# Optimization experiments

Measured on AMD Instinct MI355X. Metric: run time of the kernel, lower is better.

Reference implementation:

```python
import jax, jax.numpy as jnp
import numpy as np

E = 512      # embed_size
H = 8        # num_heads
L = 4        # num_layers
SF = 4       # sparsity_factor
F_IN = 128   # input feature dim (nn.Linear(128, embed_size))
N_CLS = 10


def setup_inputs() -> dict:
    key = jax.random.key(0)
    ks = jax.random.split(key, 14)
    B, S = 8, 1024
    s = 0.02
    inp = {
        "x": jax.random.normal(ks[0], (B, S, F_IN), jnp.float32),
        "emb_w": jax.random.normal(ks[1], (F_IN, E), jnp.float32) * s,
        "emb_b": jnp.zeros((E,), jnp.float32),
        "Wq": jax.random.normal(ks[2], (L, E, E), jnp.float32) * s,
        "Wk": jax.random.normal(ks[3], (L, E, E), jnp.float32) * s,
        "Wv": jax.random.normal(ks[4], (L, E, E), jnp.float32) * s,
        "Wo": jax.random.normal(ks[5], (L, E, E), jnp.float32) * s,
        "bq": jnp.zeros((L, E), jnp.float32),
        "bk": jnp.zeros((L, E), jnp.float32),
        "bv": jnp.zeros((L, E), jnp.float32),
        "bo": jnp.zeros((L, E), jnp.float32),
        "fc_w": jax.random.normal(ks[6], (E, N_CLS), jnp.float32) * s,
        "fc_b": jnp.zeros((N_CLS,), jnp.float32),
    }
    return inp


def _sparse_attn(h, wq, wk, wv, wo, bq, bk, bv, bo):
    # One SparseAttention layer: per-query top-k sparsified multi-head attention.
    B, S, _ = h.shape
    d = E // H
    k = max(1, S // SF)  # keep top S/sparsity_factor keys per query
    scale = 1.0 / np.sqrt(d)

    def heads(t):  # [B,S,E] -> [B,H,S,d]
        return t.reshape(B, S, H, d).transpose(0, 2, 1, 3)

    q = heads(h @ wq + bq)
    kk = heads(h @ wk + bk)
    v = heads(h @ wv + bv)

    scores = jnp.einsum('bhqd,bhkd->bhqk', q, kk) * scale  # [B,H,S,S]
    thresh = jax.lax.top_k(scores, k)[0][..., -1:]          # k-th largest per query
    scores = jnp.where(scores >= thresh, scores, jnp.float32(-1e9))
    p = jax.nn.softmax(scores, axis=-1)
    o = jnp.einsum('bhqk,bhkd->bhqd', p, v)                 # [B,H,S,d]
    o = o.transpose(0, 2, 1, 3).reshape(B, S, E)
    return o @ wo + bo


def reference(x, emb_w, emb_b, Wq, Wk, Wv, Wo, bq, bk, bv, bo, fc_w, fc_b):
    h = x @ emb_w + emb_b  # [B,S,E]
    for l in range(L):
        h = _sparse_attn(h, Wq[l], Wk[l], Wv[l], Wo[l], bq[l], bk[l], bv[l], bo[l])
    return h.mean(axis=1) @ fc_w + fc_b  # [B,10]
```

## Files before the change

### kernel.cpp

```cpp
#include <hip/hip_runtime.h>

#define EDIM 512
#define NH 8
#define HD 64
#define SEQ 1024
#define BATCH 8
#define NLAYER 4
#define KSEL 256

typedef __attribute__((ext_vector_type(8))) short short8;
typedef __attribute__((ext_vector_type(4))) float f32x4;

__device__ __forceinline__ unsigned short bf16_rne(float f) {
    unsigned u = __float_as_uint(f);
    return (unsigned short)((u + 0x7FFFu + ((u >> 16) & 1u)) >> 16);
}
__device__ __forceinline__ float bf16_tof(unsigned short h) {
    return __uint_as_float(((unsigned)h) << 16);
}
__device__ __forceinline__ void split2(float f, unsigned short& hi, unsigned short& lo) {
    hi = bf16_rne(f);
    float r = f - bf16_tof(hi);
    lo = (unsigned short)(__float_as_uint(r) >> 16);
}
__device__ __forceinline__ void split8(const float* xs, short8& hi, short8& lo) {
#pragma unroll
    for (int j = 0; j < 8; ++j) {
        unsigned short h, lw;
        split2(xs[j], h, lw);
        hi[j] = (short)h; lo[j] = (short)lw;
    }
}
__device__ __forceinline__ unsigned fmap(float s) {
    int fi = __float_as_int(s);
    return (unsigned)(fi ^ ((fi >> 31) | 0x80000000));
}
__device__ __forceinline__ float funmap(unsigned u) {
    int fi = (u & 0x80000000u) ? (int)(u ^ 0x80000000u) : (int)~u;
    return __int_as_float(fi);
}

__global__ __launch_bounds__(256) void conv_a(const float* __restrict__ A,
                                              short* __restrict__ af, int K)
{
    const int t = threadIdx.x, l = t & 63;
    const int KC = K >> 5;
    const int kc = blockIdx.x * 4 + (t >> 6);
    const int mt = blockIdx.y;
    const int m = mt * 16 + (l & 15);
    const int kb = kc * 32 + ((l >> 4) << 3);
    float4 x0 = *(const float4*)(A + (size_t)m * K + kb);
    float4 x1 = *(const float4*)(A + (size_t)m * K + kb + 4);
    float xs[8] = {x0.x, x0.y, x0.z, x0.w, x1.x, x1.y, x1.z, x1.w};
    short8 hi, lo;
    split8(xs, hi, lo);
    short* dst = af + (size_t)((mt * KC + kc) * 2) * 512 + l * 8;
    *(short8*)(dst) = hi;
    *(short8*)(dst + 512) = lo;
}

__global__ __launch_bounds__(256) void conv_wall(const float* __restrict__ Wq,
                                                 const float* __restrict__ Wk,
                                                 const float* __restrict__ Wv,
                                                 const float* __restrict__ Wo,
                                                 short* __restrict__ wf)
{
    const int z = blockIdx.z;
    const int layer = z >> 2, mm = z & 3;
    const float* W = (mm == 0 ? Wq : mm == 1 ? Wk : mm == 2 ? Wv : Wo)
                     + (size_t)layer * EDIM * EDIM;
    const int t = threadIdx.x, l = t & 63;
    const int kc = blockIdx.x * 4 + (t >> 6);
    const int nt = blockIdx.y;
    const int n = nt * 16 + (l & 15);
    const int kb = kc * 32 + ((l >> 4) << 3);
    float xs[8];
#pragma unroll
    for (int j = 0; j < 8; ++j) xs[j] = W[(size_t)(kb + j) * EDIM + n];
    short8 hi, lo;
    split8(xs, hi, lo);
    short* dst = wf + (size_t)z * 524288 + (size_t)((nt * 16 + kc) * 2) * 512 + l * 8;
    *(short8*)(dst) = hi;
    *(short8*)(dst + 512) = lo;
}

__global__ __launch_bounds__(256) void conv_w1(const float* __restrict__ W,
                                               short* __restrict__ wf, int K, int N)
{
    const int t = threadIdx.x, l = t & 63;
    const int KC = K >> 5;
    const int kc = blockIdx.x * 4 + (t >> 6);
    const int nt = blockIdx.y;
    const int n = nt * 16 + (l & 15);
    const int kb = kc * 32 + ((l >> 4) << 3);
    float xs[8];
#pragma unroll
    for (int j = 0; j < 8; ++j) xs[j] = W[(size_t)(kb + j) * N + n];
    short8 hi, lo;
    split8(xs, hi, lo);
    short* dst = wf + (size_t)((nt * KC + kc) * 2) * 512 + l * 8;
    *(short8*)(dst) = hi;
    *(short8*)(dst + 512) = lo;
}

__global__ __launch_bounds__(256, 3) void gemm_af(const short* __restrict__ af_in,
                                                  const short* __restrict__ wf,
                                                  const float* __restrict__ bias,
                                                  float* __restrict__ Cout,
                                                  short* __restrict__ af_out,
                                                  int K)
{
    __shared__ float S[128 * 68];
    const int t = threadIdx.x, l = t & 63, w = t >> 6;
    const int KC = K >> 5;
    const int mt0 = blockIdx.x * 8 + (w & 1) * 4;
    const int nt0l = (w >> 1) * 2;
    f32x4 acc[4][2] = {};

#pragma unroll 2
    for (int kc = 0; kc < KC; ++kc) {
        short8 ah[4], al[4], bh[2], bl[2];
#pragma unroll
        for (int i = 0; i < 4; ++i) {
            const short* ap = af_in + (size_t)(((mt0 + i) * KC + kc) * 2) * 512 + l * 8;
            ah[i] = *(const short8*)(ap);
            al[i] = *(const short8*)(ap + 512);
        }
#pragma unroll
        for (int j = 0; j < 2; ++j) {
            const short* bp = wf + (size_t)(((blockIdx.y * 4 + nt0l + j) * KC + kc) * 2) * 512 + l * 8;
            bh[j] = *(const short8*)(bp);
            bl[j] = *(const short8*)(bp + 512);
        }
#pragma unroll
        for (int i = 0; i < 4; ++i)
#pragma unroll
            for (int j = 0; j < 2; ++j) {
                acc[i][j] = __builtin_amdgcn_mfma_f32_16x16x32_bf16(ah[i], bh[j], acc[i][j], 0, 0, 0);
                acc[i][j] = __builtin_amdgcn_mfma_f32_16x16x32_bf16(ah[i], bl[j], acc[i][j], 0, 0, 0);
                acc[i][j] = __builtin_amdgcn_mfma_f32_16x16x32_bf16(al[i], bh[j], acc[i][j], 0, 0, 0);
            }
    }
#pragma unroll
    for (int j = 0; j < 2; ++j) {
        const int cl = (nt0l + j) * 16 + (l & 15);
        const float bv = bias[blockIdx.y * 64 + cl];
#pragma unroll
        for (int i = 0; i < 4; ++i) {
            const int rl = ((w & 1) * 4 + i) * 16 + ((l >> 4) << 2);
#pragma unroll
            for (int r = 0; r < 4; ++r) {
                const float v = acc[i][j][r] + bv;
                S[(rl + r) * 68 + cl] = v;
                Cout[(size_t)(blockIdx.x * 128 + rl + r) * EDIM + blockIdx.y * 64 + cl] = v;
            }
        }
    }
    __syncthreads();
#pragma unroll
    for (int mi = 0; mi < 2; ++mi) {
        const int mtl = w * 2 + mi;
        const int mt = blockIdx.x * 8 + mtl;
#pragma unroll
        for (int kcl = 0; kcl < 2; ++kcl) {
            const int kc = blockIdx.y * 2 + kcl;
            const float* src = &S[(mtl * 16 + (l & 15)) * 68 + kcl * 32 + ((l >> 4) << 3)];
            float4 x0 = *(const float4*)(src);
            float4 x1 = *(const float4*)(src + 4);
            float xs[8] = {x0.x, x0.y, x0.z, x0.w, x1.x, x1.y, x1.z, x1.w};
            short8 hi, lo;
            split8(xs, hi, lo);
            short* dst = af_out + (size_t)((mt * 16 + kc) * 2) * 512 + l * 8;
            *(short8*)(dst) = hi;
            *(short8*)(dst + 512) = lo;
        }
    }
}

__global__ __launch_bounds__(256, 3) void gemm_qkv(const short* __restrict__ af,
                                                   const short* __restrict__ wfl,
                                                   const float* __restrict__ bq,
                                                   const float* __restrict__ bk,
                                                   const float* __restrict__ bv,
                                                   float* __restrict__ Qout,
                                                   short* __restrict__ kf,
                                                   short* __restrict__ vf)
{
    __shared__ float S[128 * 68];
    const int y = blockIdx.y;
    const int mat = y >> 3, e = y & 7;
    const short* wfm = wfl + (size_t)mat * 524288;
    const int t = threadIdx.x, l = t & 63, w = t >> 6;
    const int KC = EDIM >> 5;
    const int mt0 = blockIdx.x * 8 + (w & 1) * 4;
    const int nt0l = (w >> 1) * 2;
    f32x4 acc[4][2] = {};

#pragma unroll 2
    for (int kc = 0; kc < KC; ++kc) {
        short8 ah[4], al[4], bh[2], bl[2];
#pragma unroll
        for (int i = 0; i < 4; ++i) {
            const short* ap = af + (size_t)(((mt0 + i) * KC + kc) * 2) * 512 + l * 8;
            ah[i] = *(const short8*)(ap);
            al[i] = *(const short8*)(ap + 512);
        }
#pragma unroll
        for (int j = 0; j < 2; ++j) {
            const short* bp = wfm + (size_t)(((e * 4 + nt0l + j) * KC + kc) * 2) * 512 + l * 8;
            bh[j] = *(const short8*)(bp);
            bl[j] = *(const short8*)(bp + 512);
        }
#pragma unroll
        for (int i = 0; i < 4; ++i)
#pragma unroll
            for (int j = 0; j < 2; ++j) {
                acc[i][j] = __builtin_amdgcn_mfma_f32_16x16x32_bf16(ah[i], bh[j], acc[i][j], 0, 0, 0);
                acc[i][j] = __builtin_amdgcn_mfma_f32_16x16x32_bf16(ah[i], bl[j], acc[i][j], 0, 0, 0);
                acc[i][j] = __builtin_amdgcn_mfma_f32_16x16x32_bf16(al[i], bh[j], acc[i][j], 0, 0, 0);
            }
    }

    if (mat == 0) {
#pragma unroll
        for (int j = 0; j < 2; ++j) {
            const int col = e * 64 + (nt0l + j) * 16 + (l & 15);
            const float bvx = bq[col];
#pragma unroll
            for (int i = 0; i < 4; ++i) {
                const int rowb = (mt0 + i) * 16 + ((l >> 4) << 2);
#pragma unroll
                for (int r = 0; r < 4; ++r)
                    Qout[(size_t)(rowb + r) * EDIM + col] = acc[i][j][r] + bvx;
            }
        }
        return;
    }

    const int STR = (mat == 1) ? 68 : 66;
    const float* bias = (mat == 1) ? bk : bv;
#pragma unroll
    for (int j = 0; j < 2; ++j) {
        const int cl = (nt0l + j) * 16 + (l & 15);
        const float bvx = bias[e * 64 + cl];
#pragma unroll
        for (int i = 0; i < 4; ++i) {
            const int rl = ((w & 1) * 4 + i) * 16 + ((l >> 4) << 2);
#pragma unroll
            for (int r = 0; r < 4; ++r)
                S[(rl + r) * STR + cl] = acc[i][j][r] + bvx;
        }
    }
    __syncthreads();

    const int b = blockIdx.x >> 3;
    const int bh2 = b * 8 + e;
    if (mat == 1) {
#pragma unroll
        for (int ki = 0; ki < 2; ++ki) {
            const int ktl = w * 2 + ki;
            const int kt = (blockIdx.x & 7) * 8 + ktl;
#pragma unroll
            for (int kc = 0; kc < 2; ++kc) {
                const float* src = &S[(ktl * 16 + (l & 15)) * 68 + kc * 32 + ((l >> 4) << 3)];
                float4 x0 = *(const float4*)(src);
                float4 x1 = *(const float4*)(src + 4);
                float xs[8] = {x0.x, x0.y, x0.z, x0.w, x1.x, x1.y, x1.z, x1.w};
                short8 hi, lo;
                split8(xs, hi, lo);
                short* dst = kf + (size_t)(((bh2 * 64 + kt) * 2 + kc) * 2) * 512 + l * 8;
                *(short8*)(dst) = hi;
                *(short8*)(dst + 512) = lo;
            }
        }
    } else {
        const int jc = (blockIdx.x & 7) * 4 + w;
#pragma unroll
        for (int n = 0; n < 4; ++n) {
            float xs[8];
#pragma unroll
            for (int j2 = 0; j2 < 8; ++j2)
                xs[j2] = S[(w * 32 + ((l >> 4) << 3) + j2) * 66 + n * 16 + (l & 15)];
            short8 hi, lo;
            split8(xs, hi, lo);
            short* dst = vf + (size_t)(((bh2 * 32 + jc) * 4 + n) * 2) * 512 + l * 8;
            *(short8*)(dst) = hi;
            *(short8*)(dst + 512) = lo;
        }
    }
}

#define SPART 65536
#define SSTG  69632

__global__ __launch_bounds__(512, 4) void attn_mfma(const float* __restrict__ Q,
                                                    const short* __restrict__ KF,
                                                    const short* __restrict__ VF,
                                                    short* __restrict__ afo)
{
    __shared__ alignas(16) unsigned char Sb[16 * 4096 + 4096 + 4352];

    const int bh = blockIdx.x, b = bh >> 3, hh = bh & 7;
    const int q0 = blockIdx.y * 16;
    const int t = threadIdx.x, l = t & 63, w = t >> 6;

    short8 aqh[2], aql[2];
    {
        const float* qp = Q + (size_t)(b * SEQ + q0 + (l & 15)) * EDIM + hh * HD + ((l >> 4) << 3);
#pragma unroll
        for (int kc = 0; kc < 2; ++kc) {
            float4 x0 = *(const float4*)(qp + kc * 32);
            float4 x1 = *(const float4*)(qp + kc * 32 + 4);
            float xs[8] = {x0.x * 0.125f, x0.y * 0.125f, x0.z * 0.125f, x0.w * 0.125f,
                           x1.x * 0.125f, x1.y * 0.125f, x1.z * 0.125f, x1.w * 0.125f};
            split8(xs, aqh[kc], aql[kc]);
        }
    }

    {
        const short* kfb = KF + (size_t)bh * 64 * 2048;
        const int rb = (l >> 4) << 2;
        for (int i = 0; i < 8; ++i) {
            const int kt = (w << 3) + i;
            const short* kp = kfb + (size_t)kt * 2048 + l * 8;
            short8 b00 = *(const short8*)(kp);
            short8 b01 = *(const short8*)(kp + 512);
            short8 b10 = *(const short8*)(kp + 1024);
            short8 b11 = *(const short8*)(kp + 1536);
            f32x4 acc = {0.f, 0.f, 0.f, 0.f};
            acc = __builtin_amdgcn_mfma_f32_16x16x32_bf16(aqh[0], b00, acc, 0, 0, 0);
            acc = __builtin_amdgcn_mfma_f32_16x16x32_bf16(aqh[0], b01, acc, 0, 0, 0);
            acc = __builtin_amdgcn_mfma_f32_16x16x32_bf16(aql[0], b00, acc, 0, 0, 0);
            acc = __builtin_amdgcn_mfma_f32_16x16x32_bf16(aqh[1], b10, acc, 0, 0, 0);
            acc = __builtin_amdgcn_mfma_f32_16x16x32_bf16(aqh[1], b11, acc, 0, 0, 0);
            acc = __builtin_amdgcn_mfma_f32_16x16x32_bf16(aql[1], b10, acc, 0, 0, 0);
            const int col = (kt << 4) + (l & 15);
            const int cg = col >> 2, wi = col & 3;
#pragma unroll
            for (int r = 0; r < 4; ++r) {
                const int row = rb + r;
                *(float*)(Sb + row * 4096 + (((cg ^ row) << 4) | (wi << 2))) = acc[r];
            }
        }
    }
    __syncthreads();

    {
        const int r0 = w << 1, r1 = r0 + 1;

        unsigned u0[16], u1[16];
#pragma unroll
        for (int n = 0; n < 4; ++n) {
            float4 s0 = *(const float4*)(Sb + r0 * 4096 + (((l + (n << 6)) ^ r0) << 4));
            float4 s1 = *(const float4*)(Sb + r1 * 4096 + (((l + (n << 6)) ^ r1) << 4));
            u0[n * 4 + 0] = fmap(s0.x); u0[n * 4 + 1] = fmap(s0.y);
            u0[n * 4 + 2] = fmap(s0.z); u0[n * 4 + 3] = fmap(s0.w);
            u1[n * 4 + 0] = fmap(s1.x); u1[n * 4 + 1] = fmap(s1.y);
            u1[n * 4 + 2] = fmap(s1.z); u1[n * 4 + 3] = fmap(s1.w);
        }

        unsigned um0 = u0[0], um1 = u1[0];
#pragma unroll
        for (int i = 1; i < 16; ++i) {
            um0 = u0[i] > um0 ? u0[i] : um0;
            um1 = u1[i] > um1 ? u1[i] : um1;
        }
#pragma unroll
        for (int off = 32; off > 0; off >>= 1) {
            unsigned o0 = __shfl_xor((int)um0, off);
            unsigned o1 = __shfl_xor((int)um1, off);
            um0 = o0 > um0 ? o0 : um0;
            um1 = o1 > um1 ? o1 : um1;
        }

        unsigned T0 = 0, T1 = 0;
        bool d0 = false, d1 = false;
        for (int bit = 31; bit >= 0; --bit) {
            const unsigned msk = 1u << bit;
            if (!d0) {
                const unsigned c0 = T0 | msk;
                if (c0 <= um0) {
                    int n0 = 0;
#pragma unroll
                    for (int i = 0; i < 16; ++i)
                        n0 += (int)__popcll(__ballot(u0[i] >= c0));
                    if (n0 >= KSEL) { T0 = c0; d0 = (n0 == KSEL); }
                }
            }
            if (!d1) {
                const unsigned c1 = T1 | msk;
                if (c1 <= um1) {
                    int n1 = 0;
#pragma unroll
                    for (int i = 0; i < 16; ++i)
                        n1 += (int)__popcll(__ballot(u1[i] >= c1));
                    if (n1 >= KSEL) { T1 = c1; d1 = (n1 == KSEL); }
                }
            }
            if (d0 & d1) break;
        }

        const float m0 = funmap(um0), m1 = funmap(um1);
        float e0[16], e1[16];
        float Z0 = 0.f, Z1 = 0.f;
#pragma unroll
        for (int i = 0; i < 16; ++i) {
            e0[i] = (u0[i] >= T0) ? __expf(funmap(u0[i]) - m0) : 0.f;
            e1[i] = (u1[i] >= T1) ? __expf(funmap(u1[i]) - m1) : 0.f;
            Z0 += e0[i];
            Z1 += e1[i];
        }
#pragma unroll
        for (int off = 32; off > 0; off >>= 1) {
            Z0 += __shfl_xor(Z0, off);
            Z1 += __shfl_xor(Z1, off);
        }
        const float zi0 = 1.0f / Z0, zi1 = 1.0f / Z1;
#pragma unroll
        for (int n = 0; n < 4; ++n) {
            const int gg = ((l + (n << 6)) >> 1);
            short4 H, L;
            unsigned short h, lw;
            split2(e0[n * 4 + 0] * zi0, h, lw); H.x = (short)h; L.x = (short)lw;
            split2(e0[n * 4 + 1] * zi0, h, lw); H.y = (short)h; L.y = (short)lw;
            split2(e0[n * 4 + 2] * zi0, h, lw); H.z = (short)h; L.z = (short)lw;
            split2(e0[n * 4 + 3] * zi0, h, lw); H.w = (short)h; L.w = (short)lw;
            unsigned char* base0 = Sb + r0 * 4096 + (((gg ^ r0) << 4) | ((l & 1) << 3));
            *(short4*)(base0) = H;
            *(short4*)(base0 + 2048) = L;
            split2(e1[n * 4 + 0] * zi1, h, lw); H.x = (short)h; L.x = (short)lw;
            split2(e1[n * 4 + 1] * zi1, h, lw); H.y = (short)h; L.y = (short)lw;
            split2(e1[n * 4 + 2] * zi1, h, lw); H.z = (short)h; L.z = (short)lw;
            split2(e1[n * 4 + 3] * zi1, h, lw); H.w = (short)h; L.w = (short)lw;
            unsigned char* base1 = Sb + r1 * 4096 + (((gg ^ r1) << 4) | ((l & 1) << 3));
            *(short4*)(base1) = H;
            *(short4*)(base1 + 2048) = L;
        }
    }
    __syncthreads();

    f32x4 oacc = {0.f, 0.f, 0.f, 0.f};
    const int cht = w & 3;
    {
        const int hf = w >> 2;
        const short* vfb = VF + (size_t)bh * 32 * 4096 + (size_t)cht * 1024;
        const int m = l & 15, g3 = l >> 4;
        for (int jc = hf * 16; jc < hf * 16 + 16; ++jc) {
            const int gg = (jc << 2) + g3;
            const unsigned char* abase = Sb + m * 4096 + ((gg ^ m) << 4);
            short8 ph = *(const short8*)(abase);
            short8 pl = *(const short8*)(abase + 2048);
            const short* vp = vfb + (size_t)jc * 4096 + l * 8;
            short8 vh = *(const short8*)(vp);
            short8 vl = *(const short8*)(vp + 512);
            oacc = __builtin_amdgcn_mfma_f32_16x16x32_bf16(ph, vh, oacc, 0, 0, 0);
            oacc = __builtin_amdgcn_mfma_f32_16x16x32_bf16(ph, vl, oacc, 0, 0, 0);
            oacc = __builtin_amdgcn_mfma_f32_16x16x32_bf16(pl, vh, oacc, 0, 0, 0);
        }
    }
    {
        float* part = (float*)(Sb + SPART);
        const int ch = l & 15, rb = (l >> 4) << 2;
        if (w >= 4) {
#pragma unroll
            for (int r = 0; r < 4; ++r)
                part[(cht * 16 + rb + r) * 16 + ch] = oacc[r];
        }
        __syncthreads();
        if (w < 4) {
            float* stage = (float*)(Sb + SSTG);
#pragma unroll
            for (int r = 0; r < 4; ++r) {
                const float v = oacc[r] + part[(cht * 16 + rb + r) * 16 + ch];
                stage[(rb + r) * 68 + cht * 16 + ch] = v;
            }
        }
        __syncthreads();
    }
    if (w < 2) {
        const float* stage = (const float*)(Sb + SSTG);
        const float* src = stage + (l & 15) * 68 + w * 32 + ((l >> 4) << 3);
        float4 x0 = *(const float4*)(src);
        float4 x1 = *(const float4*)(src + 4);
        float xs[8] = {x0.x, x0.y, x0.z, x0.w, x1.x, x1.y, x1.z, x1.w};
        short8 hi, lo;
        split8(xs, hi, lo);
        const int mt = (b * SEQ + q0) >> 4;
        const int kc = hh * 2 + w;
        short* dst = afo + (size_t)((mt * 16 + kc) * 2) * 512 + l * 8;
        *(short8*)(dst) = hi;
        *(short8*)(dst + 512) = lo;
    }
}

__global__ __launch_bounds__(256) void mean_fc(const float* __restrict__ Hf,
                                               const float* __restrict__ fcw,
                                               const float* __restrict__ fcb,
                                               float* __restrict__ out)
{
    __shared__ float hm[EDIM];
    const int b = blockIdx.x, t = threadIdx.x;
    const float* hb = Hf + (size_t)b * SEQ * EDIM;
    float s0 = 0.f, s1 = 0.f;
    for (int s = 0; s < SEQ; ++s) {
        s0 += hb[(size_t)s * EDIM + t];
        s1 += hb[(size_t)s * EDIM + t + 256];
    }
    hm[t] = s0 * (1.0f / SEQ);
    hm[t + 256] = s1 * (1.0f / SEQ);
    __syncthreads();
    if (t < 10) {
        float acc = fcb[t];
        for (int e = 0; e < EDIM; ++e) acc += hm[e] * fcw[e * 10 + t];
        out[b * 10 + t] = acc;
    }
}

extern "C" void kernel_launch(void* const* d_in, const int* in_sizes, int n_in,
                              void* d_out, int out_size, void* d_ws, size_t ws_size,
                              hipStream_t stream)
{
    const float* x     = (const float*)d_in[0];
    const float* emb_w = (const float*)d_in[1];
    const float* emb_b = (const float*)d_in[2];
    const float* Wq    = (const float*)d_in[3];
    const float* Wk    = (const float*)d_in[4];
    const float* Wv    = (const float*)d_in[5];
    const float* Wo    = (const float*)d_in[6];
    const float* bq    = (const float*)d_in[7];
    const float* bk    = (const float*)d_in[8];
    const float* bv    = (const float*)d_in[9];
    const float* bo    = (const float*)d_in[10];
    const float* fcw   = (const float*)d_in[11];
    const float* fcb   = (const float*)d_in[12];
    float* out = (float*)d_out;
    float* ws  = (float*)d_ws;

    const size_t SZ = (size_t)BATCH * SEQ * EDIM;
    float* h   = ws;
    float* q   = ws + SZ;
    short* afo = (short*)(ws + 2 * SZ);
    short* afx = (short*)(ws + 3 * SZ);
    short* wfe = afx + 4 * 1024 * 1024;
    short* kf  = (short*)(ws + 4 * SZ);
    short* vf  = (short*)(ws + 5 * SZ);
    short* afh = (short*)(ws + 6 * SZ);
    short* wf  = (short*)(ws + 7 * SZ);

    const int M = BATCH * SEQ;
    const dim3 gG(M / 128, EDIM / 64);
    const dim3 gQKV(M / 128, 3 * EDIM / 64);
    const dim3 gA(BATCH * NH, SEQ / 16);

    conv_wall<<<dim3(4, 32, 16), 256, 0, stream>>>(Wq, Wk, Wv, Wo, wf);
    conv_w1<<<dim3(1, 32), 256, 0, stream>>>(emb_w, wfe, 128, EDIM);
    conv_a<<<dim3(1, M / 16), 256, 0, stream>>>(x, afx, 128);
    gemm_af<<<gG, 256, 0, stream>>>(afx, wfe, emb_b, h, afh, 128);

    for (int l = 0; l < NLAYER; ++l) {
        const short* wfl = wf + (size_t)(4 * l) * 524288;
        gemm_qkv<<<gQKV, 256, 0, stream>>>(afh, wfl, bq + l * EDIM, bk + l * EDIM,
                                           bv + l * EDIM, q, kf, vf);
        attn_mfma<<<gA, 512, 0, stream>>>(q, kf, vf, afo);
        gemm_af<<<gG, 256, 0, stream>>>(afo, wfl + 3 * 524288, bo + l * EDIM, h, afh, EDIM);
    }
    mean_fc<<<8, 256, 0, stream>>>(h, fcw, fcb, out);
}
```

Measured before the change: 1.138 ms.

## Emit Q in split-bf16 MFMA layout, fold scale, defer softmax normalization

The 1/sqrt(d) scale is folded into the Wq weight conversion and the q bias, so the QKV GEMM writes Q directly as hi/lo bf16 fragments in MFMA layout. Attention then loads Q fragments instead of fp32 rows, removing the fp32 Q round trip and the per-block split. Softmax normalization is deferred: unnormalized exponentials are written to shared memory and the row reciprocal is applied to the output accumulator, which drops the e0/e1 register arrays and a pass over them. The fp32 hidden-state write is skipped for every GEMM except the final one, saving global stores at the cost of an extra shared-memory staging step for Q.

```diff
diff --git a/kernel.cpp b/kernel.cpp
--- a/kernel.cpp
+++ b/kernel.cpp
@@ -69,6 +69,7 @@
     const int layer = z >> 2, mm = z & 3;
     const float* W = (mm == 0 ? Wq : mm == 1 ? Wk : mm == 2 ? Wv : Wo)
                      + (size_t)layer * EDIM * EDIM;
+    const float sc = (mm == 0) ? 0.125f : 1.0f;
     const int t = threadIdx.x, l = t & 63;
     const int kc = blockIdx.x * 4 + (t >> 6);
     const int nt = blockIdx.y;
@@ -76,7 +77,7 @@
     const int kb = kc * 32 + ((l >> 4) << 3);
     float xs[8];
 #pragma unroll
-    for (int j = 0; j < 8; ++j) xs[j] = W[(size_t)(kb + j) * EDIM + n];
+    for (int j = 0; j < 8; ++j) xs[j] = W[(size_t)(kb + j) * EDIM + n] * sc;
     short8 hi, lo;
     split8(xs, hi, lo);
     short* dst = wf + (size_t)z * 524288 + (size_t)((nt * 16 + kc) * 2) * 512 + l * 8;
@@ -152,7 +153,8 @@
             for (int r = 0; r < 4; ++r) {
                 const float v = acc[i][j][r] + bv;
                 S[(rl + r) * 68 + cl] = v;
-                Cout[(size_t)(blockIdx.x * 128 + rl + r) * EDIM + blockIdx.y * 64 + cl] = v;
+                if (Cout)
+                    Cout[(size_t)(blockIdx.x * 128 + rl + r) * EDIM + blockIdx.y * 64 + cl] = v;
             }
         }
     }
@@ -182,7 +184,7 @@
                                                    const float* __restrict__ bq,
                                                    const float* __restrict__ bk,
                                                    const float* __restrict__ bv,
-                                                   float* __restrict__ Qout,
+                                                   short* __restrict__ qf,
                                                    short* __restrict__ kf,
                                                    short* __restrict__ vf)
 {
@@ -221,28 +223,13 @@
             }
     }
 
-    if (mat == 0) {
-#pragma unroll
-        for (int j = 0; j < 2; ++j) {
-            const int col = e * 64 + (nt0l + j) * 16 + (l & 15);
-            const float bvx = bq[col];
-#pragma unroll
-            for (int i = 0; i < 4; ++i) {
-                const int rowb = (mt0 + i) * 16 + ((l >> 4) << 2);
-#pragma unroll
-                for (int r = 0; r < 4; ++r)
-                    Qout[(size_t)(rowb + r) * EDIM + col] = acc[i][j][r] + bvx;
-            }
-        }
-        return;
-    }
-
-    const int STR = (mat == 1) ? 68 : 66;
-    const float* bias = (mat == 1) ? bk : bv;
+    const int STR = (mat == 2) ? 66 : 68;
+    const float* bias = mat == 0 ? bq : mat == 1 ? bk : bv;
+    const float bsc = (mat == 0) ? 0.125f : 1.0f;
 #pragma unroll
     for (int j = 0; j < 2; ++j) {
         const int cl = (nt0l + j) * 16 + (l & 15);
-        const float bvx = bias[e * 64 + cl];
+        const float bvx = bias[e * 64 + cl] * bsc;
 #pragma unroll
         for (int i = 0; i < 4; ++i) {
             const int rl = ((w & 1) * 4 + i) * 16 + ((l >> 4) << 2);
@@ -252,6 +239,28 @@
         }
     }
     __syncthreads();
+
+    if (mat == 0) {
+#pragma unroll
+        for (int mi = 0; mi < 2; ++mi) {
+            const int mtl = w * 2 + mi;
+            const int mt = blockIdx.x * 8 + mtl;
+#pragma unroll
+            for (int kcl = 0; kcl < 2; ++kcl) {
+                const int kc = e * 2 + kcl;
+                const float* src = &S[(mtl * 16 + (l & 15)) * 68 + kcl * 32 + ((l >> 4) << 3)];
+                float4 x0 = *(const float4*)(src);
+                float4 x1 = *(const float4*)(src + 4);
+                float xs[8] = {x0.x, x0.y, x0.z, x0.w, x1.x, x1.y, x1.z, x1.w};
+                short8 hi, lo;
+                split8(xs, hi, lo);
+                short* dst = qf + (size_t)((mt * 16 + kc) * 2) * 512 + l * 8;
+                *(short8*)(dst) = hi;
+                *(short8*)(dst + 512) = lo;
+            }
+        }
+        return;
+    }
 
     const int b = blockIdx.x >> 3;
     const int bh2 = b * 8 + e;
@@ -292,29 +301,26 @@
 
 #define SPART 65536
 #define SSTG  69632
-
-__global__ __launch_bounds__(512, 4) void attn_mfma(const float* __restrict__ Q,
+#define SZINV 73984
+
+__global__ __launch_bounds__(512, 4) void attn_mfma(const short* __restrict__ QF,
                                                     const short* __restrict__ KF,
                                                     const short* __restrict__ VF,
                                                     short* __restrict__ afo)
 {
-    __shared__ alignas(16) unsigned char Sb[16 * 4096 + 4096 + 4352];
+    __shared__ alignas(16) unsigned char Sb[16 * 4096 + 4096 + 4352 + 64];
 
     const int bh = blockIdx.x, b = bh >> 3, hh = bh & 7;
     const int q0 = blockIdx.y * 16;
     const int t = threadIdx.x, l = t & 63, w = t >> 6;
+    const int qmt = (b * SEQ + q0) >> 4;
 
     short8 aqh[2], aql[2];
-    {
-        const float* qp = Q + (size_t)(b * SEQ + q0 + (l & 15)) * EDIM + hh * HD + ((l >> 4) << 3);
-#pragma unroll
-        for (int kc = 0; kc < 2; ++kc) {
-            float4 x0 = *(const float4*)(qp + kc * 32);
-            float4 x1 = *(const float4*)(qp + kc * 32 + 4);
-            float xs[8] = {x0.x * 0.125f, x0.y * 0.125f, x0.z * 0.125f, x0.w * 0.125f,
-                           x1.x * 0.125f, x1.y * 0.125f, x1.z * 0.125f, x1.w * 0.125f};
-            split8(xs, aqh[kc], aql[kc]);
-        }
+#pragma unroll
+    for (int kc = 0; kc < 2; ++kc) {
+        const short* qp = QF + (size_t)((qmt * 16 + hh * 2 + kc) * 2) * 512 + l * 8;
+        aqh[kc] = *(const short8*)(qp);
+        aql[kc] = *(const short8*)(qp + 512);
     }
 
     {
@@ -401,40 +407,51 @@
         }
 
         const float m0 = funmap(um0), m1 = funmap(um1);
-        float e0[16], e1[16];
         float Z0 = 0.f, Z1 = 0.f;
-#pragma unroll
-        for (int i = 0; i < 16; ++i) {
-            e0[i] = (u0[i] >= T0) ? __expf(funmap(u0[i]) - m0) : 0.f;
-            e1[i] = (u1[i] >= T1) ? __expf(funmap(u1[i]) - m1) : 0.f;
-            Z0 += e0[i];
-            Z1 += e1[i];
-        }
-#pragma unroll
-        for (int off = 32; off > 0; off >>= 1) {
-            Z0 += __shfl_xor(Z0, off);
-            Z1 += __shfl_xor(Z1, off);
-        }
-        const float zi0 = 1.0f / Z0, zi1 = 1.0f / Z1;
 #pragma unroll
         for (int n = 0; n < 4; ++n) {
             const int gg = ((l + (n << 6)) >> 1);
             short4 H, L;
             unsigned short h, lw;
-            split2(e0[n * 4 + 0] * zi0, h, lw); H.x = (short)h; L.x = (short)lw;
-            split2(e0[n * 4 + 1] * zi0, h, lw); H.y = (short)h; L.y = (short)lw;
-            split2(e0[n * 4 + 2] * zi0, h, lw); H.z = (short)h; L.z = (short)lw;
-            split2(e0[n * 4 + 3] * zi0, h, lw); H.w = (short)h; L.w = (short)lw;
-            unsigned char* base0 = Sb + r0 * 4096 + (((gg ^ r0) << 4) | ((l & 1) << 3));
-            *(short4*)(base0) = H;
-            *(short4*)(base0 + 2048) = L;
-            split2(e1[n * 4 + 0] * zi1, h, lw); H.x = (short)h; L.x = (short)lw;
-            split2(e1[n * 4 + 1] * zi1, h, lw); H.y = (short)h; L.y = (short)lw;
-            split2(e1[n * 4 + 2] * zi1, h, lw); H.z = (short)h; L.z = (short)lw;
-            split2(e1[n * 4 + 3] * zi1, h, lw); H.w = (short)h; L.w = (short)lw;
-            unsigned char* base1 = Sb + r1 * 4096 + (((gg ^ r1) << 4) | ((l & 1) << 3));
-            *(short4*)(base1) = H;
-            *(short4*)(base1 + 2048) = L;
+            {
+                float e0 = (u0[n * 4 + 0] >= T0) ? __expf(funmap(u0[n * 4 + 0]) - m0) : 0.f;
+                float e1 = (u0[n * 4 + 1] >= T0) ? __expf(funmap(u0[n * 4 + 1]) - m0) : 0.f;
+                float e2 = (u0[n * 4 + 2] >= T0) ? __expf(funmap(u0[n * 4 + 2]) - m0) : 0.f;
+                float e3 = (u0[n * 4 + 3] >= T0) ? __expf(funmap(u0[n * 4 + 3]) - m0) : 0.f;
+                Z0 += (e0 + e1) + (e2 + e3);
+                split2(e0, h, lw); H.x = (short)h; L.x = (short)lw;
+                split2(e1, h, lw); H.y = (short)h; L.y = (short)lw;
+                split2(e2, h, lw); H.z = (short)h; L.z = (short)lw;
+                split2(e3, h, lw); H.w = (short)h; L.w = (short)lw;
+                unsigned char* base0 = Sb + r0 * 4096 + (((gg ^ r0) << 4) | ((l & 1) << 3));
+                *(short4*)(base0) = H;
+                *(short4*)(base0 + 2048) = L;
+            }
+            {
+                float e0 = (u1[n * 4 + 0] >= T1) ? __expf(funmap(u1[n * 4 + 0]) - m1) : 0.f;
+                float e1 = (u1[n * 4 + 1] >= T1) ? __expf(funmap(u1[n * 4 + 1]) - m1) : 0.f;
+                float e2 = (u1[n * 4 + 2] >= T1) ? __expf(funmap(u1[n * 4 + 2]) - m1) : 0.f;
+                float e3 = (u1[n * 4 + 3] >= T1) ? __expf(funmap(u1[n * 4 + 3]) - m1) : 0.f;
+                Z1 += (e0 + e1) + (e2 + e3);
+                split2(e0, h, lw); H.x = (short)h; L.x = (short)lw;
+                split2(e1, h, lw); H.y = (short)h; L.y = (short)lw;
+                split2(e2, h, lw); H.z = (short)h; L.z = (short)lw;
+                split2(e3, h, lw); H.w = (short)h; L.w = (short)lw;
+                unsigned char* base1 = Sb + r1 * 4096 + (((gg ^ r1) << 4) | ((l & 1) << 3));
+                *(short4*)(base1) = H;
+                *(short4*)(base1 + 2048) = L;
+            }
+        }
+
+#pragma unroll
+        for (int off = 32; off > 0; off >>= 1) {
+            Z0 += __shfl_xor(Z0, off);
+            Z1 += __shfl_xor(Z1, off);
+        }
+        if (l == 0) {
+            float* zin = (float*)(Sb + SZINV);
+            zin[r0] = 1.0f / Z0;
+            zin[r1] = 1.0f / Z1;
         }
     }
     __syncthreads();
@@ -460,6 +477,7 @@
     }
     {
         float* part = (float*)(Sb + SPART);
+        const float* zin = (const float*)(Sb + SZINV);
         const int ch = l & 15, rb = (l >> 4) << 2;
         if (w >= 4) {
 #pragma unroll
@@ -471,7 +489,7 @@
             float* stage = (float*)(Sb + SSTG);
 #pragma unroll
             for (int r = 0; r < 4; ++r) {
-                const float v = oacc[r] + part[(cht * 16 + rb + r) * 16 + ch];
+                const float v = (oacc[r] + part[(cht * 16 + rb + r) * 16 + ch]) * zin[rb + r];
                 stage[(rb + r) * 68 + cht * 16 + ch] = v;
             }
         }
@@ -485,9 +503,8 @@
         float xs[8] = {x0.x, x0.y, x0.z, x0.w, x1.x, x1.y, x1.z, x1.w};
         short8 hi, lo;
         split8(xs, hi, lo);
-        const int mt = (b * SEQ + q0) >> 4;
         const int kc = hh * 2 + w;
-        short* dst = afo + (size_t)((mt * 16 + kc) * 2) * 512 + l * 8;
+        short* dst = afo + (size_t)((qmt * 16 + kc) * 2) * 512 + l * 8;
         *(short8*)(dst) = hi;
         *(short8*)(dst + 512) = lo;
     }
@@ -538,7 +555,7 @@
 
     const size_t SZ = (size_t)BATCH * SEQ * EDIM;
     float* h   = ws;
-    float* q   = ws + SZ;
+    short* qf  = (short*)(ws + SZ);
     short* afo = (short*)(ws + 2 * SZ);
     short* afx = (short*)(ws + 3 * SZ);
     short* wfe = afx + 4 * 1024 * 1024;
@@ -555,14 +572,15 @@
     conv_wall<<<dim3(4, 32, 16), 256, 0, stream>>>(Wq, Wk, Wv, Wo, wf);
     conv_w1<<<dim3(1, 32), 256, 0, stream>>>(emb_w, wfe, 128, EDIM);
     conv_a<<<dim3(1, M / 16), 256, 0, stream>>>(x, afx, 128);
-    gemm_af<<<gG, 256, 0, stream>>>(afx, wfe, emb_b, h, afh, 128);
+    gemm_af<<<gG, 256, 0, stream>>>(afx, wfe, emb_b, nullptr, afh, 128);
 
     for (int l = 0; l < NLAYER; ++l) {
         const short* wfl = wf + (size_t)(4 * l) * 524288;
         gemm_qkv<<<gQKV, 256, 0, stream>>>(afh, wfl, bq + l * EDIM, bk + l * EDIM,
-                                           bv + l * EDIM, q, kf, vf);
-        attn_mfma<<<gA, 512, 0, stream>>>(q, kf, vf, afo);
-        gemm_af<<<gG, 256, 0, stream>>>(afo, wfl + 3 * 524288, bo + l * EDIM, h, afh, EDIM);
+                                           bv + l * EDIM, qf, kf, vf);
+        attn_mfma<<<gA, 512, 0, stream>>>(qf, kf, vf, afo);
+        gemm_af<<<gG, 256, 0, stream>>>(afo, wfl + 3 * 524288, bo + l * EDIM,
+                                        (l == NLAYER - 1) ? h : nullptr, afh, EDIM);
     }
     mean_fc<<<8, 256, 0, stream>>>(h, fcw, fcb, out);
 }
```

Result: faster. 1.084 ms (-4.8%).
